# Performance work log

Measured on AMD Instinct MI355X. Metric: run time of the kernel, lower is better.

The kernel has to match this reference:

```python
import jax, jax.numpy as jnp
import numpy as np

EPS = 1e-6

def _normalize(x):
    # x / sqrt(max(||x||^2, eps)) -- matches torch clamp_min on squared norm
    n2 = jnp.sum(x * x, axis=-1, keepdims=True)
    return x / jnp.sqrt(jnp.maximum(n2, EPS))

def setup_inputs() -> dict:
    key = jax.random.key(0)
    k1, k2, k3, k4 = jax.random.split(key, 4)
    B, N, M, D = 2, 4096, 4096, 256
    state_dim, out_dim = 2 * D, 512
    em1 = jax.random.normal(k1, (B, N, D), dtype=jnp.float32)
    em2 = jax.random.normal(k2, (B, M, D), dtype=jnp.float32)
    # fc params (torch Linear init: U(-1/sqrt(in), 1/sqrt(in)))
    bound = 1.0 / np.sqrt(state_dim)
    W = jax.random.uniform(k3, (out_dim, state_dim), minval=-bound, maxval=bound, dtype=jnp.float32)
    b = jax.random.uniform(k4, (out_dim,), minval=-bound, maxval=bound, dtype=jnp.float32)
    return {"em1": em1, "em2": em2, "W": W, "b": b}

def reference(em1, em2, W, b):
    # cosine similarity = normalized GEMM (same math as broadcast mul+sum)
    s = jnp.einsum('bnd,bmd->bnm', _normalize(em1), _normalize(em2))  # [B,N,M]
    soft = jax.nn.softmax(s, axis=-1)
    x = jnp.einsum('bnm,bmd->bnd', soft, em2)                          # [B,N,D]
    emb = jnp.concatenate([em1, x], axis=-1)                           # [B,N,2D]
    h = jax.nn.relu(emb @ W.T + b)                                     # [B,N,out_dim]
    return h
```

## Files before the change

kernel.cpp:

```cpp
#include <hip/hip_runtime.h>

#define BATCH 2
#define NQ    4096
#define MK    4096
#define DD    256
#define ODIM  512
#define SDIM  512
#define NROWS (BATCH * NQ)
#define BM    64
#define BK    64
#define MSPLIT 4
#define MCHUNK (MK / MSPLIT)
#define NKT    (MCHUNK / BK)
#define XSPLIT (BATCH * NQ * DD)

#define NCH_E1 (NROWS * DD / 8)
#define NCH_K  NCH_E1
#define NCH_V  NCH_E1
#define NCH_W  (ODIM * SDIM / 8)
#define RN_BLOCKS 4096

typedef short bf16x8 __attribute__((ext_vector_type(8)));
typedef float f32x16 __attribute__((ext_vector_type(16)));

__device__ __forceinline__ float bf2f(unsigned short h) {
    unsigned int u = ((unsigned int)h) << 16;
    float f;
    __builtin_memcpy(&f, &u, 4);
    return f;
}
__device__ __forceinline__ unsigned short f2bf(float f) {
    unsigned int u;
    __builtin_memcpy(&u, &f, 4);
    u = (u + 0x7FFFu + ((u >> 16) & 1u)) >> 16;
    return (unsigned short)u;
}
union frag_cast { uint4 u; bf16x8 b; unsigned short h[8]; };
__device__ __forceinline__ bf16x8 ldg_frag(const unsigned short* p) {
    frag_cast c;
    c.u = *(const uint4*)p;
    return c.b;
}
__device__ __forceinline__ void load_lds16(const unsigned short* g, unsigned short* l) {
    __builtin_amdgcn_global_load_lds(
        (const __attribute__((address_space(1))) void*)g,
        (__attribute__((address_space(3))) void*)l, 16, 0, 0);
}

__global__ void prep_kernel(const float* em1, const float* em2, const float* W,
                            float* rn, unsigned short* e1sw, unsigned short* ksw,
                            unsigned short* vsw, unsigned short* wsw) {
    int bid = blockIdx.x;
    if (bid < RN_BLOCKS) {
        int row  = bid * 4 + (threadIdx.x >> 6);
        int lane = threadIdx.x & 63;
        const float* src = (row < NROWS) ? em1 + (size_t)row * DD
                                         : em2 + (size_t)(row - NROWS) * DD;
        float4 v = *(const float4*)(src + lane * 4);
        float ss = v.x * v.x + v.y * v.y + v.z * v.z + v.w * v.w;
#pragma unroll
        for (int off = 1; off < 64; off <<= 1) ss += __shfl_xor(ss, off, 64);
        if (lane == 0) rn[row] = rsqrtf(fmaxf(ss, 1e-6f));
        return;
    }
    int cg = (bid - RN_BLOCKS) * 256 + threadIdx.x;
    if (cg < NCH_E1 + NCH_K) {
        const float* src;
        unsigned short* dst;
        int c0;
        if (cg < NCH_E1) { src = em1; dst = e1sw; c0 = cg; }
        else             { src = em2; dst = ksw;  c0 = cg - NCH_E1; }
        int g = c0 >> 10, c = c0 & 1023;
        int r31 = c & 31;
        int k0  = (c >> 5) * 8;
        const float* sp = src + (size_t)(g * 32 + r31) * DD + k0;
        float4 a = *(const float4*)sp;
        float4 b = *(const float4*)(sp + 4);
        ushort4 o1, o2;
        o1.x = f2bf(a.x); o1.y = f2bf(a.y); o1.z = f2bf(a.z); o1.w = f2bf(a.w);
        o2.x = f2bf(b.x); o2.y = f2bf(b.y); o2.z = f2bf(b.z); o2.w = f2bf(b.w);
        *(ushort4*)(dst + (size_t)c0 * 8)     = o1;
        *(ushort4*)(dst + (size_t)c0 * 8 + 4) = o2;
    } else if (cg < NCH_E1 + NCH_K + NCH_V) {
        int c0 = cg - (NCH_E1 + NCH_K);
        int b   = c0 >> 17;
        int r   = c0 & 131071;
        int dg  = r >> 14;
        int rr  = r & 16383;
        int oct = rr >> 5;
        int d31 = rr & 31;
        const float* sp = em2 + (size_t)(b * MK + oct * 8) * DD + dg * 32 + d31;
        ushort4 o1, o2;
        o1.x = f2bf(sp[0 * DD]); o1.y = f2bf(sp[1 * DD]);
        o1.z = f2bf(sp[2 * DD]); o1.w = f2bf(sp[3 * DD]);
        o2.x = f2bf(sp[4 * DD]); o2.y = f2bf(sp[5 * DD]);
        o2.z = f2bf(sp[6 * DD]); o2.w = f2bf(sp[7 * DD]);
        *(ushort4*)(vsw + (size_t)c0 * 8)     = o1;
        *(ushort4*)(vsw + (size_t)c0 * 8 + 4) = o2;
    } else {
        int c0 = cg - (NCH_E1 + NCH_K + NCH_V);
        if (c0 >= NCH_W) return;
        int g = c0 >> 11, c = c0 & 2047;
        int c31 = c & 31;
        int k0  = (c >> 5) * 8;
        const float* sp = W + (size_t)(g * 32 + c31) * SDIM + k0;
        float4 a = *(const float4*)sp;
        float4 b = *(const float4*)(sp + 4);
        ushort4 o1, o2;
        o1.x = f2bf(a.x); o1.y = f2bf(a.y); o1.z = f2bf(a.z); o1.w = f2bf(a.w);
        o2.x = f2bf(b.x); o2.y = f2bf(b.y); o2.z = f2bf(b.z); o2.w = f2bf(b.w);
        *(ushort4*)(wsw + (size_t)c0 * 8)     = o1;
        *(ushort4*)(wsw + (size_t)c0 * 8 + 4) = o2;
    }
}

__global__ __launch_bounds__(256, 2)
void flash_kernel(const unsigned short* e1sw, const unsigned short* ksw,
                  const unsigned short* vsw, const float* rn,
                  unsigned short* Xp, float* lbuf) {
    __shared__ unsigned short Ks[16384];
    __shared__ unsigned short Ps[BM * 72];
    __shared__ float ls[2][BM];
    int tid = threadIdx.x, lane = tid & 63, w = tid >> 6;
    int l31 = lane & 31, lhalf = lane >> 5;
    int wr = w & 1, wc = w >> 1;
    int bid    = blockIdx.x;
    int mchunk = bid & 3;
    int rowblk = bid >> 2;
    int batch  = rowblk >> 6;
    int r0     = rowblk * BM;

    const unsigned short* qbase =
        e1sw + (size_t)(rowblk * 2 + wr) * 8192 + lhalf * 256 + l31 * 8;
    bf16x8 qf[16];
#pragma unroll
    for (int s = 0; s < 16; s++) qf[s] = ldg_frag(qbase + s * 512);

    float rqv[16];
#pragma unroll
    for (int i = 0; i < 16; i++) {
        int m = (i & 3) + 8 * (i >> 2) + 4 * lhalf;
        rqv[i] = rn[r0 + wr * 32 + m];
    }
    const float* rnk = rn + NROWS + batch * MK + mchunk * MCHUNK;

    const unsigned short* kchunk = ksw + (size_t)(batch * 128 + mchunk * 32) * 8192;
    const unsigned short* vbase  = vsw + (size_t)batch * 1048576 +
                                   (size_t)(mchunk * 128) * 256;

    f32x16 xacc[4];
#pragma unroll
    for (int t = 0; t < 4; t++)
#pragma unroll
        for (int i = 0; i < 16; i++) xacc[t][i] = 0.f;
    float lpart[16];
#pragma unroll
    for (int i = 0; i < 16; i++) lpart[i] = 0.f;

#pragma unroll
    for (int it = 0; it < 8; it++)
        load_lds16(kchunk + it * 2048 + tid * 8, &Ks[it * 2048 + tid * 8]);

    for (int kt = 0; kt < NKT; kt++) {
        __syncthreads();
        if (kt > 0) {
            const unsigned short* vp = vbase + (size_t)((kt - 1) * 8) * 256 +
                                       lhalf * 256 + l31 * 8;
#pragma unroll
            for (int ks = 0; ks < 4; ks++) {
                frag_cast ac;
                ac.u = *(const uint4*)&Ps[(wr * 32 + l31) * 72 + ks * 16 + lhalf * 8];
#pragma unroll
                for (int nt = 0; nt < 4; nt++) {
                    bf16x8 bf = ldg_frag(vp + (size_t)(wc * 4 + nt) * 131072 + ks * 512);
                    xacc[nt] = __builtin_amdgcn_mfma_f32_32x32x16_bf16(ac.b, bf, xacc[nt], 0, 0, 0);
                }
            }
        }
        f32x16 sA, sB;
#pragma unroll
        for (int i = 0; i < 16; i++) { sA[i] = 0.f; sB[i] = 0.f; }
        const unsigned short* kb = &Ks[wc * 8192 + lhalf * 256 + l31 * 8];
#pragma unroll
        for (int s = 0; s < 16; s += 2) {
            bf16x8 b0 = ldg_frag(kb + s * 512);
            bf16x8 b1 = ldg_frag(kb + (s + 1) * 512);
            sA = __builtin_amdgcn_mfma_f32_32x32x16_bf16(qf[s],     b0, sA, 0, 0, 0);
            sB = __builtin_amdgcn_mfma_f32_32x32x16_bf16(qf[s + 1], b1, sB, 0, 0, 0);
        }
        float rk = rnk[kt * BK + wc * 32 + l31];
        __syncthreads();
        {
            int ktn = (kt + 1 < NKT) ? kt + 1 : kt;
            const unsigned short* ksrc = kchunk + (size_t)ktn * 16384;
#pragma unroll
            for (int it = 0; it < 8; it++)
                load_lds16(ksrc + it * 2048 + tid * 8, &Ks[it * 2048 + tid * 8]);
        }
#pragma unroll
        for (int i = 0; i < 16; i++) {
            float p = __expf((sA[i] + sB[i]) * rqv[i] * rk - 1.0f);
            unsigned short pb = f2bf(p);
            lpart[i] += bf2f(pb);
            int m = wr * 32 + (i & 3) + 8 * (i >> 2) + 4 * lhalf;
            Ps[m * 72 + wc * 32 + l31] = pb;
        }
    }
    __syncthreads();
    {
        const unsigned short* vp = vbase + (size_t)((NKT - 1) * 8) * 256 +
                                   lhalf * 256 + l31 * 8;
#pragma unroll
        for (int ks = 0; ks < 4; ks++) {
            frag_cast ac;
            ac.u = *(const uint4*)&Ps[(wr * 32 + l31) * 72 + ks * 16 + lhalf * 8];
#pragma unroll
            for (int nt = 0; nt < 4; nt++) {
                bf16x8 bf = ldg_frag(vp + (size_t)(wc * 4 + nt) * 131072 + ks * 512);
                xacc[nt] = __builtin_amdgcn_mfma_f32_32x32x16_bf16(ac.b, bf, xacc[nt], 0, 0, 0);
            }
        }
    }

#pragma unroll
    for (int i = 0; i < 16; i++) {
        float v = lpart[i];
#pragma unroll
        for (int off = 1; off < 32; off <<= 1) v += __shfl_xor(v, off, 64);
        if (l31 == 0) {
            int m = wr * 32 + (i & 3) + 8 * (i >> 2) + 4 * lhalf;
            ls[wc][m] = v;
        }
    }
    __syncthreads();
    if (tid < BM)
        lbuf[(size_t)mchunk * NROWS + r0 + tid] = ls[0][tid] + ls[1][tid];

    unsigned short* xout = Xp + (size_t)mchunk * XSPLIT +
                           (size_t)(rowblk * 2 + wr) * 8192;
#pragma unroll
    for (int nt = 0; nt < 4; nt++) {
        int dcol = wc * 128 + nt * 32 + l31;
        int cbase = (dcol >> 3) * 256 + (dcol & 7);
#pragma unroll
        for (int i = 0; i < 16; i++) {
            int m = (i & 3) + 8 * (i >> 2) + 4 * lhalf;
            xout[cbase + m * 8] = f2bf(xacc[nt][i]);
        }
    }
}

__global__ void reduce_kernel(const unsigned short* Xp, const float* lbuf,
                              unsigned short* xnsw) {
    int cg  = blockIdx.x * 256 + threadIdx.x;
    int row = (cg >> 10) * 32 + (cg & 31);
    float l = lbuf[row] + lbuf[NROWS + row] +
              lbuf[2 * NROWS + row] + lbuf[3 * NROWS + row];
    float rinv = 1.0f / l;
    const unsigned short* p = Xp + (size_t)cg * 8;
    frag_cast p0, p1, p2, p3, u;
    p0.u = *(const uint4*)p;
    p1.u = *(const uint4*)(p + (size_t)XSPLIT);
    p2.u = *(const uint4*)(p + 2 * (size_t)XSPLIT);
    p3.u = *(const uint4*)(p + 3 * (size_t)XSPLIT);
#pragma unroll
    for (int j = 0; j < 8; j++) {
        float f = bf2f(p0.h[j]) + bf2f(p1.h[j]) + bf2f(p2.h[j]) + bf2f(p3.h[j]);
        u.h[j] = f2bf(f * rinv);
    }
    *(uint4*)(xnsw + (size_t)cg * 8) = u.u;
}

__global__ __launch_bounds__(256, 4)
void final_gemm(const unsigned short* e1sw, const unsigned short* xnsw,
                const unsigned short* wsw, const float* bias, float* out) {
    int tid = threadIdx.x, lane = tid & 63, w = tid >> 6;
    int l31 = lane & 31, lhalf = lane >> 5;
    int wr = w & 1, wc = w >> 1;
    int bid = blockIdx.x;
    int rb = bid & 127, cb = bid >> 7;
    int gA = rb * 2 + wr;
    int gB = cb * 2 + wc;

    f32x16 acc;
#pragma unroll
    for (int i = 0; i < 16; i++) acc[i] = 0.f;

    const unsigned short* abase = e1sw + (size_t)gA * 8192 + lhalf * 256 + l31 * 8;
    const unsigned short* xbase = xnsw + (size_t)gA * 8192 + lhalf * 256 + l31 * 8;
    const unsigned short* bbase = wsw  + (size_t)gB * 16384 + lhalf * 256 + l31 * 8;

    for (int kk = 0; kk < 32; kk++) {
        bf16x8 afr = (kk < 16) ? ldg_frag(abase + kk * 512)
                               : ldg_frag(xbase + (kk - 16) * 512);
        bf16x8 bfr = ldg_frag(bbase + kk * 512);
        acc = __builtin_amdgcn_mfma_f32_32x32x16_bf16(afr, bfr, acc, 0, 0, 0);
    }

    int col = gB * 32 + l31;
    float bb = bias[col];
#pragma unroll
    for (int i = 0; i < 16; i++) {
        int row = gA * 32 + (i & 3) + 8 * (i >> 2) + 4 * lhalf;
        float v = acc[i] + bb;
        v = v > 0.f ? v : 0.f;
        out[(size_t)row * ODIM + col] = v;
    }
}

extern "C" void kernel_launch(void* const* d_in, const int* in_sizes, int n_in,
                              void* d_out, int out_size, void* d_ws, size_t ws_size,
                              hipStream_t stream) {
    const float* em1  = (const float*)d_in[0];
    const float* em2  = (const float*)d_in[1];
    const float* W    = (const float*)d_in[2];
    const float* bias = (const float*)d_in[3];
    float* out = (float*)d_out;

    char* ws = (char*)d_ws;
    unsigned short* e1sw = (unsigned short*)ws;
    unsigned short* ksw  = e1sw + (size_t)NROWS * DD;
    unsigned short* vsw  = ksw  + (size_t)NROWS * DD;
    unsigned short* wsw  = vsw  + (size_t)BATCH * DD * MK;
    unsigned short* Xp   = wsw  + (size_t)ODIM * SDIM;
    unsigned short* xnsw = Xp   + 4 * (size_t)XSPLIT;
    float* lbuf = (float*)(xnsw + (size_t)NROWS * DD);
    float* rn   = lbuf + 4 * (size_t)NROWS;

    const int swz_blocks = (NCH_E1 + NCH_K + NCH_V + NCH_W + 255) / 256;
    prep_kernel<<<RN_BLOCKS + swz_blocks, 256, 0, stream>>>(
        em1, em2, W, rn, e1sw, ksw, vsw, wsw);
    flash_kernel<<<(NROWS / BM) * MSPLIT, 256, 0, stream>>>(e1sw, ksw, vsw, rn, Xp, lbuf);
    reduce_kernel<<<NCH_E1 / 256, 256, 0, stream>>>(Xp, lbuf, xnsw);
    final_gemm<<<(NROWS / 64) * (ODIM / 64), 256, 0, stream>>>(
        e1sw, xnsw, wsw, bias, out);
}
```

Baseline: 158.9 us.

## Stage V tiles through LDS and drop K prefetch pipelining in flash kernel

Each iteration now loads both the K tile and the V tile into shared memory, then syncs, computes S and P, syncs again and runs the PV MFMAs from LDS instead of reading V fragments straight from global memory. The software pipeline that overlapped the next K load and the previous PV product is removed, so each step is serialized with an extra barrier. Block indexing is also remapped so that consecutive blocks share an M chunk, which may improve L2 reuse of K/V. LDS use roughly doubles (adds 32KB), which may reduce occupancy at two blocks per CU, and load latency is no longer hidden.

```diff
diff --git a/kernel.cpp b/kernel.cpp
--- a/kernel.cpp
+++ b/kernel.cpp
@@ -119,14 +119,15 @@
                   const unsigned short* vsw, const float* rn,
                   unsigned short* Xp, float* lbuf) {
     __shared__ unsigned short Ks[16384];
+    __shared__ unsigned short Vs[16384];
     __shared__ unsigned short Ps[BM * 72];
     __shared__ float ls[2][BM];
     int tid = threadIdx.x, lane = tid & 63, w = tid >> 6;
     int l31 = lane & 31, lhalf = lane >> 5;
     int wr = w & 1, wc = w >> 1;
     int bid    = blockIdx.x;
-    int mchunk = bid & 3;
-    int rowblk = bid >> 2;
+    int mchunk = bid >> 7;
+    int rowblk = bid & 127;
     int batch  = rowblk >> 6;
     int r0     = rowblk * BM;
 
@@ -157,26 +158,19 @@
 #pragma unroll
     for (int i = 0; i < 16; i++) lpart[i] = 0.f;
 
-#pragma unroll
-    for (int it = 0; it < 8; it++)
-        load_lds16(kchunk + it * 2048 + tid * 8, &Ks[it * 2048 + tid * 8]);
-
     for (int kt = 0; kt < NKT; kt++) {
         __syncthreads();
-        if (kt > 0) {
-            const unsigned short* vp = vbase + (size_t)((kt - 1) * 8) * 256 +
-                                       lhalf * 256 + l31 * 8;
-#pragma unroll
-            for (int ks = 0; ks < 4; ks++) {
-                frag_cast ac;
-                ac.u = *(const uint4*)&Ps[(wr * 32 + l31) * 72 + ks * 16 + lhalf * 8];
-#pragma unroll
-                for (int nt = 0; nt < 4; nt++) {
-                    bf16x8 bf = ldg_frag(vp + (size_t)(wc * 4 + nt) * 131072 + ks * 512);
-                    xacc[nt] = __builtin_amdgcn_mfma_f32_32x32x16_bf16(ac.b, bf, xacc[nt], 0, 0, 0);
-                }
-            }
-        }
+        {
+            const unsigned short* ksrc = kchunk + (size_t)kt * 16384;
+#pragma unroll
+            for (int it = 0; it < 8; it++)
+                load_lds16(ksrc + it * 2048 + tid * 8, &Ks[it * 2048 + tid * 8]);
+            const unsigned short* vsrc = vbase + (size_t)(kt * 8) * 256;
+#pragma unroll
+            for (int dg = 0; dg < 8; dg++)
+                load_lds16(vsrc + (size_t)dg * 131072 + tid * 8, &Vs[dg * 2048 + tid * 8]);
+        }
+        __syncthreads();
         f32x16 sA, sB;
 #pragma unroll
         for (int i = 0; i < 16; i++) { sA[i] = 0.f; sB[i] = 0.f; }
@@ -189,14 +183,6 @@
             sB = __builtin_amdgcn_mfma_f32_32x32x16_bf16(qf[s + 1], b1, sB, 0, 0, 0);
         }
         float rk = rnk[kt * BK + wc * 32 + l31];
-        __syncthreads();
-        {
-            int ktn = (kt + 1 < NKT) ? kt + 1 : kt;
-            const unsigned short* ksrc = kchunk + (size_t)ktn * 16384;
-#pragma unroll
-            for (int it = 0; it < 8; it++)
-                load_lds16(ksrc + it * 2048 + tid * 8, &Ks[it * 2048 + tid * 8]);
-        }
 #pragma unroll
         for (int i = 0; i < 16; i++) {
             float p = __expf((sA[i] + sB[i]) * rqv[i] * rk - 1.0f);
@@ -205,18 +191,14 @@
             int m = wr * 32 + (i & 3) + 8 * (i >> 2) + 4 * lhalf;
             Ps[m * 72 + wc * 32 + l31] = pb;
         }
-    }
-    __syncthreads();
-    {
-        const unsigned short* vp = vbase + (size_t)((NKT - 1) * 8) * 256 +
-                                   lhalf * 256 + l31 * 8;
+        __syncthreads();
 #pragma unroll
         for (int ks = 0; ks < 4; ks++) {
             frag_cast ac;
             ac.u = *(const uint4*)&Ps[(wr * 32 + l31) * 72 + ks * 16 + lhalf * 8];
 #pragma unroll
             for (int nt = 0; nt < 4; nt++) {
-                bf16x8 bf = ldg_frag(vp + (size_t)(wc * 4 + nt) * 131072 + ks * 512);
+                bf16x8 bf = ldg_frag(&Vs[((wc * 4 + nt) * 8 + ks * 2 + lhalf) * 256 + l31 * 8]);
                 xacc[nt] = __builtin_amdgcn_mfma_f32_32x32x16_bf16(ac.b, bf, xacc[nt], 0, 0, 0);
             }
         }
```

Measured after the change: 142.2 us. 1.12x faster.
